# Performance work log

Hardware: AMD Instinct MI355X
Metric: run time of the kernel (lower is better)

## Reference

```python
import jax, jax.numpy as jnp
import numpy as np

N, E, G = 50000, 800000, 512
D_IN, HID, E_DIM = 128, 128, 128
NEG_SLOPE = 0.2


def setup_inputs() -> dict:
    key = jax.random.key(0)
    ks = iter(jax.random.split(key, 40))
    nrm = lambda shape, s: jax.random.normal(next(ks), shape, jnp.float32) * s
    lin = lambda i, o: nrm((i, o), 1.0 / np.sqrt(i))
    inp = {
        "x": jax.random.randint(next(ks), (N, 9), 0, 119),
        "edge_index": jax.random.randint(next(ks), (2, E), 0, N),
        "edge_attr": jax.random.randint(next(ks), (E, 3), 0, 5),
        "batch": jnp.sort(jax.random.randint(next(ks), (N,), 0, G)),
        # OGB-style encoders: sum of per-feature embeddings
        "atom_emb": nrm((9, 128, D_IN), 0.1),
        "bond_emb": nrm((3, 8, E_DIM), 0.1),
        # GATv2 layer 1 (in=D_IN)
        "W1l": lin(D_IN, HID), "b1l": jnp.zeros((HID,), jnp.float32),
        "W1r": lin(D_IN, HID), "b1r": jnp.zeros((HID,), jnp.float32),
        "W1e": lin(E_DIM, HID), "att1": nrm((HID,), 1.0 / np.sqrt(HID)),
        "bias1": jnp.zeros((HID,), jnp.float32),
        # GATv2 layer 2 (in=HID)
        "W2l": lin(HID, HID), "b2l": jnp.zeros((HID,), jnp.float32),
        "W2r": lin(HID, HID), "b2r": jnp.zeros((HID,), jnp.float32),
        "W2e": lin(E_DIM, HID), "att2": nrm((HID,), 1.0 / np.sqrt(HID)),
        "bias2": jnp.zeros((HID,), jnp.float32),
        # readout linear
        "Wout": lin(HID, 1), "bout": jnp.zeros((1,), jnp.float32),
    }
    return inp


def _segment_softmax(scores, seg, n):
    m = jax.ops.segment_max(scores, seg, num_segments=n)
    ex = jnp.exp(scores - m[seg])
    s = jax.ops.segment_sum(ex, seg, num_segments=n)
    return ex / s[seg]


def _add_self_loops(edge_index, edge_attr):
    # PyG add_self_loops with fill_value='mean': loop attr = mean of incoming edge_attr
    dst = edge_index[1]
    cnt = jax.ops.segment_sum(jnp.ones((E,), edge_attr.dtype), dst, num_segments=N)
    mean_attr = jax.ops.segment_sum(edge_attr, dst, num_segments=N) / jnp.maximum(cnt, 1.0)[:, None]
    loop = jnp.arange(N)
    ei = jnp.concatenate([edge_index, jnp.stack([loop, loop])], axis=1)
    ea = jnp.concatenate([edge_attr, mean_attr], axis=0)
    return ei, ea


def _gatv2(h, src, dst, e_emb, Wl, bl, Wr, br, We, att, bias):
    hl = h @ Wl + bl                      # [N, HID] source transform
    hr = h @ Wr + br                      # [N, HID] target transform
    z = jax.nn.leaky_relu(hl[src] + hr[dst] + e_emb @ We, NEG_SLOPE)  # [E', HID]
    alpha = _segment_softmax(z @ att, dst, N)                          # [E']
    out = jax.ops.segment_sum(alpha[:, None] * hl[src], dst, num_segments=N)
    return out + bias


def reference(x, edge_index, edge_attr, batch, atom_emb, bond_emb,
              W1l, b1l, W1r, b1r, W1e, att1, bias1,
              W2l, b2l, W2r, b2r, W2e, att2, bias2, Wout, bout):
    # encoders: sum of per-feature embedding lookups
    h = jnp.sum(atom_emb[jnp.arange(9)[None, :], x], axis=1)        # [N, D_IN]
    ea = jnp.sum(bond_emb[jnp.arange(3)[None, :], edge_attr], axis=1)  # [E, E_DIM]
    ei, ea = _add_self_loops(edge_index, ea)
    src, dst = ei[0], ei[1]
    h = _gatv2(h, src, dst, ea, W1l, b1l, W1r, b1r, W1e, att1, bias1)
    h = jax.nn.relu(h)
    h = _gatv2(h, src, dst, ea, W2l, b2l, W2r, b2r, W2e, att2, bias2)
    # global mean pool over graphs
    cnt = jax.ops.segment_sum(jnp.ones((N,), h.dtype), batch, num_segments=G)
    g = jax.ops.segment_sum(h, batch, num_segments=G) / jnp.maximum(cnt, 1.0)[:, None]
    # dropout is identity in eval mode
    return jax.nn.sigmoid(g @ Wout + bout)                           # [G, 1]
```

## Files before the change

### kernel.cpp

```cpp
#include <hip/hip_runtime.h>
#include <hip/hip_bf16.h>
#include <math.h>


typedef unsigned int uint;

#define THREADS 256
#define LOG2E 1.4426950408889634f
#define SRC_MASK 0x7fffffu

__global__ void atom_kernel(const int* __restrict__ x, const float* __restrict__ atom_emb,
                            float* __restrict__ h, int n) {
  int idx = blockIdx.x * blockDim.x + threadIdx.x;
  int node = idx >> 7, d = idx & 127;
  if (node >= n) return;
  float s = 0.f;
#pragma unroll
  for (int f = 0; f < 9; f++) {
    int v = x[node * 9 + f];
    s += atom_emb[(f * 128 + v) * 128 + d];
  }
  h[idx] = s;
}

__global__ void edge_hist_kernel(const int* __restrict__ ei, const int* __restrict__ ea,
                                 uint* __restrict__ cnt, uint* __restrict__ hist, int E_) {
  int e = blockIdx.x * blockDim.x + threadIdx.x;
  if (e >= E_) return;
  int dst = ei[E_ + e];
  int a0 = ea[e * 3 + 0], a1 = ea[e * 3 + 1], a2 = ea[e * 3 + 2];
  atomicAdd(&cnt[dst], 1u);
  atomicAdd(&hist[dst * 24 + a0], 1u);
  atomicAdd(&hist[dst * 24 + 8 + a1], 1u);
  atomicAdd(&hist[dst * 24 + 16 + a2], 1u);
}

__global__ __launch_bounds__(256) void scanA_kernel(const uint* __restrict__ cnt,
                                                    uint* __restrict__ off,
                                                    uint* __restrict__ bsum, int n) {
  __shared__ uint sc[256];
  int t = threadIdx.x;
  int base = blockIdx.x * 1024 + t * 4;
  uint v[4];
#pragma unroll
  for (int i = 0; i < 4; i++) v[i] = (base + i < n) ? cnt[base + i] : 0u;
  uint s = v[0] + v[1] + v[2] + v[3];
  sc[t] = s;
  __syncthreads();
  for (int o = 1; o < 256; o <<= 1) {
    uint w = (t >= o) ? sc[t - o] : 0u;
    __syncthreads();
    sc[t] += w;
    __syncthreads();
  }
  uint excl = sc[t] - s;
  uint r = excl;
#pragma unroll
  for (int i = 0; i < 4; i++) {
    if (base + i < n) off[base + i] = r;
    r += v[i];
  }
  if (t == 255) bsum[blockIdx.x] = sc[t];
}

__global__ __launch_bounds__(256) void scanB_kernel(const uint* __restrict__ bsum,
                                                    uint* __restrict__ bpre, int nb) {
  __shared__ uint sc[256];
  int t = threadIdx.x;
  uint s = (t < nb) ? bsum[t] : 0u;
  sc[t] = s;
  __syncthreads();
  for (int o = 1; o < 256; o <<= 1) {
    uint w = (t >= o) ? sc[t - o] : 0u;
    __syncthreads();
    sc[t] += w;
    __syncthreads();
  }
  if (t < nb) bpre[t] = sc[t] - s;
}

__global__ void scanC_kernel(uint* __restrict__ off, const uint* __restrict__ bpre, int n,
                             int E_) {
  int i = blockIdx.x * blockDim.x + threadIdx.x;
  if (i < n) off[i] += bpre[i >> 10];
  if (i == 0) off[n] = (uint)E_;
}

__global__ void scatter_kernel(const int* __restrict__ ei, const int* __restrict__ ea,
                               const uint* __restrict__ off, uint* __restrict__ fill,
                               uint* __restrict__ sorted, int E_) {
  int e = blockIdx.x * blockDim.x + threadIdx.x;
  if (e >= E_) return;
  int src = ei[e], dst = ei[E_ + e];
  uint pos = off[dst] + atomicAdd(&fill[dst], 1u);
  uint pk = ((uint)src & SRC_MASK) | ((uint)ea[e * 3 + 0] << 23) |
            ((uint)ea[e * 3 + 1] << 26) | ((uint)ea[e * 3 + 2] << 29);
  sorted[pos] = pk;
}

__global__ void table_kernel(const float* __restrict__ bond_emb, const float* __restrict__ W1e,
                             const float* __restrict__ W2e, float* __restrict__ tab1,
                             float* __restrict__ tab2) {
  __shared__ float row[128];
  int b = blockIdx.x;
  int j = (b < 24) ? b : b - 24;
  const float* We = (b < 24) ? W1e : W2e;
  float* tab = (b < 24) ? tab1 : tab2;
  row[threadIdx.x] = bond_emb[j * 128 + threadIdx.x];
  __syncthreads();
  float acc = 0.f;
#pragma unroll 4
  for (int k = 0; k < 128; k++) acc += row[k] * We[k * 128 + threadIdx.x];
  tab[j * 128 + threadIdx.x] = acc;
}

__global__ __launch_bounds__(256) void lin2_kernel(
    const float* __restrict__ h, const float* __restrict__ Wl, const float* __restrict__ bl,
    const float* __restrict__ Wr, const float* __restrict__ br,
    float* __restrict__ hl, float* __restrict__ hr, int n) {
  __shared__ float hs[32][132];
  int r0 = blockIdx.x * 32;
  for (int i = threadIdx.x; i < 32 * 128; i += 256) {
    int r = i >> 7, c = i & 127;
    int gr = r0 + r;
    hs[r][c] = (gr < n) ? h[gr * 128 + c] : 0.f;
  }
  __syncthreads();
  int col = threadIdx.x & 127;
  int half = threadIdx.x >> 7;
  float accl[16], accr[16];
  float bvl = bl[col], bvr = br[col];
#pragma unroll
  for (int i = 0; i < 16; i++) { accl[i] = bvl; accr[i] = bvr; }
  for (int k = 0; k < 128; k += 4) {
    float wl[4], wr[4];
#pragma unroll
    for (int kk = 0; kk < 4; kk++) {
      wl[kk] = Wl[(k + kk) * 128 + col];
      wr[kk] = Wr[(k + kk) * 128 + col];
    }
#pragma unroll
    for (int i = 0; i < 16; i++) {
      float4 hv = *(const float4*)&hs[half * 16 + i][k];
      accl[i] += hv.x * wl[0] + hv.y * wl[1] + hv.z * wl[2] + hv.w * wl[3];
      accr[i] += hv.x * wr[0] + hv.y * wr[1] + hv.z * wr[2] + hv.w * wr[3];
    }
  }
#pragma unroll
  for (int i = 0; i < 16; i++) {
    int gr = r0 + half * 16 + i;
    if (gr < n) {
      hl[gr * 128 + col] = accl[i];
      hr[gr * 128 + col] = accr[i];
    }
  }
}

__global__ __launch_bounds__(256) void attn_kernel(
    const float* __restrict__ hl, const float* __restrict__ hr,
    const uint* __restrict__ off, const uint* __restrict__ sorted,
    const uint* __restrict__ cnt, const uint* __restrict__ hist,
    const float* __restrict__ tab, const float* __restrict__ att,
    const float* __restrict__ bias, float* __restrict__ out, int n, int do_relu) {
  __shared__ float tabs[24][128];
  __shared__ float atts[128];
  for (int i = threadIdx.x; i < 24 * 128; i += 256) tabs[i >> 7][i & 127] = tab[i];
  if (threadIdx.x < 128) atts[threadIdx.x] = att[threadIdx.x] * LOG2E;
  __syncthreads();
  int wave = threadIdx.x >> 6, lane = threadIdx.x & 63;
  int node = blockIdx.x * 4 + wave;
  if (node >= n) return;
  int d = lane * 2;

  float2 hrv = *(const float2*)&hr[node * 128 + d];
  float2 hlo = *(const float2*)&hl[node * 128 + d];
  float2 av = make_float2(atts[d], atts[d + 1]);

  float2 ep = make_float2(0.f, 0.f);
  uint c = cnt[node];
  if (c) {
#pragma unroll
    for (int j = 0; j < 24; j++) {
      float f = (float)hist[node * 24 + j];
      float2 tv = *(const float2*)&tabs[j][d];
      ep.x += f * tv.x;
      ep.y += f * tv.y;
    }
    float inv = 1.0f / (float)c;
    ep.x *= inv;
    ep.y *= inv;
  }

  auto score_of = [&](float2 hls, float2 epv) -> float {
    float tx = hls.x + hrv.x + epv.x;
    float ty = hls.y + hrv.y + epv.y;
    tx = tx > 0.f ? tx : 0.2f * tx;
    ty = ty > 0.f ? ty : 0.2f * ty;
    float p = tx * av.x + ty * av.y;
#pragma unroll
    for (int o = 32; o > 0; o >>= 1) p += __shfl_xor(p, o);
    return p;
  };
  auto eproj_of = [&](uint pk) -> float2 {
    int a0 = (pk >> 23) & 7, a1 = (pk >> 26) & 7, a2 = (pk >> 29) & 7;
    float2 t0 = *(const float2*)&tabs[a0][d];
    float2 t1 = *(const float2*)&tabs[8 + a1][d];
    float2 t2 = *(const float2*)&tabs[16 + a2][d];
    return make_float2(t0.x + t1.x + t2.x, t0.y + t1.y + t2.y);
  };

  float m = score_of(hlo, ep);
  float s = 1.0f;
  float2 acc = hlo;

  uint e0 = off[node], e1 = off[node + 1];
  for (uint e = e0; e < e1; e += 8) {
    uint pk[8];
    float2 hv[8];
    float sc[8], p[8];
#pragma unroll
    for (int i = 0; i < 8; i++) {
      uint ee = e + (uint)i;
      pk[i] = sorted[ee < e1 ? ee : e1 - 1];
    }
#pragma unroll
    for (int i = 0; i < 8; i++) hv[i] = *(const float2*)&hl[(pk[i] & SRC_MASK) * 128 + d];
#pragma unroll
    for (int i = 0; i < 8; i++) sc[i] = score_of(hv[i], eproj_of(pk[i]));
#pragma unroll
    for (int i = 0; i < 8; i++)
      if (e + (uint)i >= e1) sc[i] = -INFINITY;
    float m8 = sc[0];
#pragma unroll
    for (int i = 1; i < 8; i++) m8 = fmaxf(m8, sc[i]);
    float mn = fmaxf(m, m8);
    float corr = exp2f(m - mn);
#pragma unroll
    for (int i = 0; i < 8; i++) p[i] = exp2f(sc[i] - mn);
    float ps = 0.f;
    float2 pa = make_float2(0.f, 0.f);
#pragma unroll
    for (int i = 0; i < 8; i++) {
      ps += p[i];
      pa.x += p[i] * hv[i].x;
      pa.y += p[i] * hv[i].y;
    }
    s = s * corr + ps;
    acc.x = acc.x * corr + pa.x;
    acc.y = acc.y * corr + pa.y;
    m = mn;
  }

  float inv = 1.0f / s;
  float2 o;
  o.x = acc.x * inv + bias[d];
  o.y = acc.y * inv + bias[d + 1];
  if (do_relu) {
    o.x = fmaxf(o.x, 0.f);
    o.y = fmaxf(o.y, 0.f);
  }
  *(float2*)&out[node * 128 + d] = o;
}

#define POOL_CHUNK 128
__global__ void pool_kernel(const float* __restrict__ h, const int* __restrict__ batch,
                            float* __restrict__ pool, uint* __restrict__ cntg, int n) {
  int d = threadIdx.x;
  int i0 = blockIdx.x * POOL_CHUNK;
  if (i0 >= n) return;
  int i1 = min(i0 + POOL_CHUNK, n);
  int g = batch[i0];
  float s = 0.f;
  uint c = 0;
  for (int i = i0; i < i1; i++) {
    int gi = batch[i];
    if (gi != g) {
      atomicAdd(&pool[g * 128 + d], s);
      if (d == 0) atomicAdd(&cntg[g], c);
      g = gi;
      s = 0.f;
      c = 0;
    }
    s += h[i * 128 + d];
    c++;
  }
  atomicAdd(&pool[g * 128 + d], s);
  if (d == 0) atomicAdd(&cntg[g], c);
}

__global__ void out_kernel(const float* __restrict__ pool, const uint* __restrict__ cntg,
                           const float* __restrict__ Wout, const float* __restrict__ bout,
                           float* __restrict__ out, int g_) {
  int wave = threadIdx.x >> 6, lane = threadIdx.x & 63;
  int g = blockIdx.x * 4 + wave;
  if (g >= g_) return;
  int d = lane * 2;
  float2 pv = *(const float2*)&pool[g * 128 + d];
  float2 wv = *(const float2*)&Wout[d];
  float p = pv.x * wv.x + pv.y * wv.y;
#pragma unroll
  for (int o = 32; o > 0; o >>= 1) p += __shfl_xor(p, o);
  if (lane == 0) {
    uint c = cntg[g];
    float cf = (float)(c ? c : 1u);
    float v = p / cf + bout[0];
    out[g] = 1.f / (1.f + expf(-v));
  }
}

extern "C" void kernel_launch(void* const* d_in, const int* in_sizes, int n_in,
                              void* d_out, int out_size, void* d_ws, size_t ws_size,
                              hipStream_t stream) {
  const int* x          = (const int*)d_in[0];
  const int* edge_index = (const int*)d_in[1];
  const int* edge_attr  = (const int*)d_in[2];
  const int* batch      = (const int*)d_in[3];
  const float* atom_emb = (const float*)d_in[4];
  const float* bond_emb = (const float*)d_in[5];
  const float* W1l = (const float*)d_in[6];
  const float* b1l = (const float*)d_in[7];
  const float* W1r = (const float*)d_in[8];
  const float* b1r = (const float*)d_in[9];
  const float* W1e = (const float*)d_in[10];
  const float* att1 = (const float*)d_in[11];
  const float* bias1 = (const float*)d_in[12];
  const float* W2l = (const float*)d_in[13];
  const float* b2l = (const float*)d_in[14];
  const float* W2r = (const float*)d_in[15];
  const float* b2r = (const float*)d_in[16];
  const float* W2e = (const float*)d_in[17];
  const float* att2 = (const float*)d_in[18];
  const float* bias2 = (const float*)d_in[19];
  const float* Wout = (const float*)d_in[20];
  const float* bout = (const float*)d_in[21];
  float* out = (float*)d_out;

  const int N = in_sizes[0] / 9;
  const int E = in_sizes[1] / 2;
  const int G = out_size;
  const int NB = (N + 1023) / 1024;

  char* w = (char*)d_ws;
  auto alloc = [&](size_t bytes) -> char* {
    char* p = w;
    w += (bytes + 255) & ~(size_t)255;
    return p;
  };
  float* h0     = (float*)alloc((size_t)N * 128 * 4);
  float* hl     = (float*)alloc((size_t)N * 128 * 4);
  float* hr     = (float*)alloc((size_t)N * 128 * 4);
  uint* cnt     = (uint*)alloc((size_t)N * 4);
  uint* off     = (uint*)alloc((size_t)(N + 1) * 4);
  uint* fill    = (uint*)alloc((size_t)N * 4);
  uint* hist    = (uint*)alloc((size_t)N * 24 * 4);
  uint* sorted  = (uint*)alloc((size_t)E * 4);
  float* tab1   = (float*)alloc(24 * 128 * 4);
  float* tab2   = (float*)alloc(24 * 128 * 4);
  float* pool   = (float*)alloc((size_t)G * 128 * 4);
  uint* cntg    = (uint*)alloc((size_t)G * 4);
  uint* bsum    = (uint*)alloc((size_t)NB * 4);
  uint* bpre    = (uint*)alloc((size_t)NB * 4);

  hipMemsetAsync(cnt, 0, (size_t)N * 4, stream);
  hipMemsetAsync(fill, 0, (size_t)N * 4, stream);
  hipMemsetAsync(hist, 0, (size_t)N * 24 * 4, stream);
  hipMemsetAsync(pool, 0, (size_t)G * 128 * 4, stream);
  hipMemsetAsync(cntg, 0, (size_t)G * 4, stream);

  table_kernel<<<48, 128, 0, stream>>>(bond_emb, W1e, W2e, tab1, tab2);
  atom_kernel<<<(N * 128 + THREADS - 1) / THREADS, THREADS, 0, stream>>>(x, atom_emb, h0, N);
  edge_hist_kernel<<<(E + THREADS - 1) / THREADS, THREADS, 0, stream>>>(edge_index, edge_attr,
                                                                        cnt, hist, E);
  scanA_kernel<<<NB, 256, 0, stream>>>(cnt, off, bsum, N);
  scanB_kernel<<<1, 256, 0, stream>>>(bsum, bpre, NB);
  scanC_kernel<<<(N + THREADS - 1) / THREADS, THREADS, 0, stream>>>(off, bpre, N, E);
  scatter_kernel<<<(E + THREADS - 1) / THREADS, THREADS, 0, stream>>>(edge_index, edge_attr, off,
                                                                      fill, sorted, E);
  lin2_kernel<<<(N + 31) / 32, 256, 0, stream>>>(h0, W1l, b1l, W1r, b1r, hl, hr, N);
  attn_kernel<<<(N + 3) / 4, 256, 0, stream>>>(hl, hr, off, sorted, cnt, hist, tab1, att1, bias1,
                                               h0, N, 1);
  lin2_kernel<<<(N + 31) / 32, 256, 0, stream>>>(h0, W2l, b2l, W2r, b2r, hl, hr, N);
  attn_kernel<<<(N + 3) / 4, 256, 0, stream>>>(hl, hr, off, sorted, cnt, hist, tab2, att2, bias2,
                                               h0, N, 0);
  pool_kernel<<<(N + POOL_CHUNK - 1) / POOL_CHUNK, 128, 0, stream>>>(h0, batch, pool, cntg, N);
  out_kernel<<<(G + 3) / 4, 256, 0, stream>>>(pool, cntg, Wout, bout, out, G);
}
```

Baseline: 784.9 us.

## Split wavefront into four edge groups with float4 lanes in GATv2 attention

The attention kernel now splits each 64-lane wave into four 16-lane groups. Each group covers the 128 features with float4x2 per lane and handles a different edge, two per iteration. Partial online-softmax states are merged with cross-group shuffles at the end, which cuts the per-edge 64-lane reduction to four shuffle steps and widens the gathers. Separately, the in-degree count array and its atomics are dropped, and degree is recomputed from the attribute histogram. This adds a merge epilogue and more registers per lane.

Measured after the change: 727.7 us. 1.08x faster.

```diff
diff --git a/kernel.cpp b/kernel.cpp
--- a/kernel.cpp
+++ b/kernel.cpp
@@ -7,7 +7,29 @@
 
 #define THREADS 256
 #define LOG2E 1.4426950408889634f
+#define NEGM -1e30f
 #define SRC_MASK 0x7fffffu
+
+__device__ inline float4 f4add(float4 x, float4 y) {
+  return make_float4(x.x + y.x, x.y + y.y, x.z + y.z, x.w + y.w);
+}
+__device__ inline float4 f4fma(float c, float4 x, float4 y) {
+  return make_float4(fmaf(c, x.x, y.x), fmaf(c, x.y, y.y), fmaf(c, x.z, y.z),
+                     fmaf(c, x.w, y.w));
+}
+__device__ inline float4 f4scale(float4 x, float c) {
+  return make_float4(x.x * c, x.y * c, x.z * c, x.w * c);
+}
+__device__ inline float lrelu_dot(float4 z, float4 a) {
+  float r = (z.x > 0.f ? z.x : 0.2f * z.x) * a.x;
+  r += (z.y > 0.f ? z.y : 0.2f * z.y) * a.y;
+  r += (z.z > 0.f ? z.z : 0.2f * z.z) * a.z;
+  r += (z.w > 0.f ? z.w : 0.2f * z.w) * a.w;
+  return r;
+}
+__device__ inline float4 f4relu(float4 x) {
+  return make_float4(fmaxf(x.x, 0.f), fmaxf(x.y, 0.f), fmaxf(x.z, 0.f), fmaxf(x.w, 0.f));
+}
 
 __global__ void atom_kernel(const int* __restrict__ x, const float* __restrict__ atom_emb,
                             float* __restrict__ h, int n) {
@@ -24,18 +46,17 @@
 }
 
 __global__ void edge_hist_kernel(const int* __restrict__ ei, const int* __restrict__ ea,
-                                 uint* __restrict__ cnt, uint* __restrict__ hist, int E_) {
+                                 uint* __restrict__ hist, int E_) {
   int e = blockIdx.x * blockDim.x + threadIdx.x;
   if (e >= E_) return;
   int dst = ei[E_ + e];
   int a0 = ea[e * 3 + 0], a1 = ea[e * 3 + 1], a2 = ea[e * 3 + 2];
-  atomicAdd(&cnt[dst], 1u);
   atomicAdd(&hist[dst * 24 + a0], 1u);
   atomicAdd(&hist[dst * 24 + 8 + a1], 1u);
   atomicAdd(&hist[dst * 24 + 16 + a2], 1u);
 }
 
-__global__ __launch_bounds__(256) void scanA_kernel(const uint* __restrict__ cnt,
+__global__ __launch_bounds__(256) void scanA_kernel(const uint* __restrict__ hist,
                                                     uint* __restrict__ off,
                                                     uint* __restrict__ bsum, int n) {
   __shared__ uint sc[256];
@@ -43,7 +64,16 @@
   int base = blockIdx.x * 1024 + t * 4;
   uint v[4];
 #pragma unroll
-  for (int i = 0; i < 4; i++) v[i] = (base + i < n) ? cnt[base + i] : 0u;
+  for (int i = 0; i < 4; i++) {
+    uint d = 0;
+    int idx = base + i;
+    if (idx < n) {
+      const uint4* hp = (const uint4*)&hist[idx * 24];
+      uint4 h0 = hp[0], h1 = hp[1];
+      d = h0.x + h0.y + h0.z + h0.w + h1.x + h1.y + h1.z + h1.w;
+    }
+    v[i] = d;
+  }
   uint s = v[0] + v[1] + v[2] + v[3];
   sc[t] = s;
   __syncthreads();
@@ -53,8 +83,7 @@
     sc[t] += w;
     __syncthreads();
   }
-  uint excl = sc[t] - s;
-  uint r = excl;
+  uint r = sc[t] - s;
 #pragma unroll
   for (int i = 0; i < 4; i++) {
     if (base + i < n) off[base + i] = r;
@@ -159,107 +188,126 @@
 __global__ __launch_bounds__(256) void attn_kernel(
     const float* __restrict__ hl, const float* __restrict__ hr,
     const uint* __restrict__ off, const uint* __restrict__ sorted,
-    const uint* __restrict__ cnt, const uint* __restrict__ hist,
-    const float* __restrict__ tab, const float* __restrict__ att,
-    const float* __restrict__ bias, float* __restrict__ out, int n, int do_relu) {
+    const uint* __restrict__ hist, const float* __restrict__ tab,
+    const float* __restrict__ att, const float* __restrict__ bias,
+    float* __restrict__ out, int n, int do_relu) {
   __shared__ float tabs[24][128];
-  __shared__ float atts[128];
   for (int i = threadIdx.x; i < 24 * 128; i += 256) tabs[i >> 7][i & 127] = tab[i];
-  if (threadIdx.x < 128) atts[threadIdx.x] = att[threadIdx.x] * LOG2E;
   __syncthreads();
   int wave = threadIdx.x >> 6, lane = threadIdx.x & 63;
   int node = blockIdx.x * 4 + wave;
   if (node >= n) return;
-  int d = lane * 2;
-
-  float2 hrv = *(const float2*)&hr[node * 128 + d];
-  float2 hlo = *(const float2*)&hl[node * 128 + d];
-  float2 av = make_float2(atts[d], atts[d + 1]);
-
-  float2 ep = make_float2(0.f, 0.f);
-  uint c = cnt[node];
+  int g = lane >> 4;
+  int dq = (lane & 15) * 8;
+
+  const float* hrp = &hr[(size_t)node * 128 + dq];
+  const float* hlp = &hl[(size_t)node * 128 + dq];
+  float4 hr0 = *(const float4*)hrp, hr1 = *(const float4*)(hrp + 4);
+  float4 hl0 = *(const float4*)hlp, hl1 = *(const float4*)(hlp + 4);
+  float4 at0 = f4scale(*(const float4*)&att[dq], LOG2E);
+  float4 at1 = f4scale(*(const float4*)&att[dq + 4], LOG2E);
+
+  float4 ep0 = make_float4(0.f, 0.f, 0.f, 0.f), ep1 = ep0;
+  uint c = 0;
+#pragma unroll
+  for (int j = 0; j < 24; j++) {
+    uint hc = hist[node * 24 + j];
+    if (j < 8) c += hc;
+    if (hc) {
+      float f = (float)hc;
+      ep0 = f4fma(f, *(const float4*)&tabs[j][dq], ep0);
+      ep1 = f4fma(f, *(const float4*)&tabs[j][dq + 4], ep1);
+    }
+  }
   if (c) {
-#pragma unroll
-    for (int j = 0; j < 24; j++) {
-      float f = (float)hist[node * 24 + j];
-      float2 tv = *(const float2*)&tabs[j][d];
-      ep.x += f * tv.x;
-      ep.y += f * tv.y;
-    }
-    float inv = 1.0f / (float)c;
-    ep.x *= inv;
-    ep.y *= inv;
-  }
-
-  auto score_of = [&](float2 hls, float2 epv) -> float {
-    float tx = hls.x + hrv.x + epv.x;
-    float ty = hls.y + hrv.y + epv.y;
-    tx = tx > 0.f ? tx : 0.2f * tx;
-    ty = ty > 0.f ? ty : 0.2f * ty;
-    float p = tx * av.x + ty * av.y;
-#pragma unroll
-    for (int o = 32; o > 0; o >>= 1) p += __shfl_xor(p, o);
+    float ic = 1.f / (float)c;
+    ep0 = f4scale(ep0, ic);
+    ep1 = f4scale(ep1, ic);
+  }
+
+  auto redscore = [&](float4 z0, float4 z1) -> float {
+    float p = lrelu_dot(z0, at0) + lrelu_dot(z1, at1);
+    p += __shfl_xor(p, 1);
+    p += __shfl_xor(p, 2);
+    p += __shfl_xor(p, 4);
+    p += __shfl_xor(p, 8);
     return p;
   };
-  auto eproj_of = [&](uint pk) -> float2 {
-    int a0 = (pk >> 23) & 7, a1 = (pk >> 26) & 7, a2 = (pk >> 29) & 7;
-    float2 t0 = *(const float2*)&tabs[a0][d];
-    float2 t1 = *(const float2*)&tabs[8 + a1][d];
-    float2 t2 = *(const float2*)&tabs[16 + a2][d];
-    return make_float2(t0.x + t1.x + t2.x, t0.y + t1.y + t2.y);
-  };
-
-  float m = score_of(hlo, ep);
-  float s = 1.0f;
-  float2 acc = hlo;
+
+  float sself = redscore(f4add(f4add(hl0, hr0), ep0), f4add(f4add(hl1, hr1), ep1));
+
+  float m, s;
+  float4 a0, a1;
+  if (g == 0) {
+    m = sself; s = 1.f; a0 = hl0; a1 = hl1;
+  } else {
+    m = NEGM; s = 0.f;
+    a0 = make_float4(0.f, 0.f, 0.f, 0.f); a1 = a0;
+  }
 
   uint e0 = off[node], e1 = off[node + 1];
-  for (uint e = e0; e < e1; e += 8) {
-    uint pk[8];
-    float2 hv[8];
-    float sc[8], p[8];
-#pragma unroll
-    for (int i = 0; i < 8; i++) {
-      uint ee = e + (uint)i;
-      pk[i] = sorted[ee < e1 ? ee : e1 - 1];
-    }
-#pragma unroll
-    for (int i = 0; i < 8; i++) hv[i] = *(const float2*)&hl[(pk[i] & SRC_MASK) * 128 + d];
-#pragma unroll
-    for (int i = 0; i < 8; i++) sc[i] = score_of(hv[i], eproj_of(pk[i]));
-#pragma unroll
-    for (int i = 0; i < 8; i++)
-      if (e + (uint)i >= e1) sc[i] = -INFINITY;
-    float m8 = sc[0];
-#pragma unroll
-    for (int i = 1; i < 8; i++) m8 = fmaxf(m8, sc[i]);
-    float mn = fmaxf(m, m8);
+  for (uint base = e0; base < e1; base += 8) {
+    uint eA = base + (uint)g, eB = eA + 4u;
+    uint iA = eA < e1 ? eA : e1 - 1;
+    uint iB = eB < e1 ? eB : e1 - 1;
+    uint pkA = sorted[iA], pkB = sorted[iB];
+    const float* pa = &hl[(size_t)(pkA & SRC_MASK) * 128 + dq];
+    const float* pb = &hl[(size_t)(pkB & SRC_MASK) * 128 + dq];
+    float4 hA0 = *(const float4*)pa, hA1 = *(const float4*)(pa + 4);
+    float4 hB0 = *(const float4*)pb, hB1 = *(const float4*)(pb + 4);
+    int a0A = (pkA >> 23) & 7, a1A = (pkA >> 26) & 7, a2A = (pkA >> 29) & 7;
+    int a0B = (pkB >> 23) & 7, a1B = (pkB >> 26) & 7, a2B = (pkB >> 29) & 7;
+    float4 eA0 = f4add(f4add(*(const float4*)&tabs[a0A][dq], *(const float4*)&tabs[8 + a1A][dq]),
+                       *(const float4*)&tabs[16 + a2A][dq]);
+    float4 eA1 = f4add(f4add(*(const float4*)&tabs[a0A][dq + 4],
+                             *(const float4*)&tabs[8 + a1A][dq + 4]),
+                       *(const float4*)&tabs[16 + a2A][dq + 4]);
+    float4 eB0 = f4add(f4add(*(const float4*)&tabs[a0B][dq], *(const float4*)&tabs[8 + a1B][dq]),
+                       *(const float4*)&tabs[16 + a2B][dq]);
+    float4 eB1 = f4add(f4add(*(const float4*)&tabs[a0B][dq + 4],
+                             *(const float4*)&tabs[8 + a1B][dq + 4]),
+                       *(const float4*)&tabs[16 + a2B][dq + 4]);
+    float scA = redscore(f4add(f4add(hA0, hr0), eA0), f4add(f4add(hA1, hr1), eA1));
+    float scB = redscore(f4add(f4add(hB0, hr0), eB0), f4add(f4add(hB1, hr1), eB1));
+    if (eA >= e1) scA = NEGM;
+    if (eB >= e1) scB = NEGM;
+    float mn = fmaxf(m, fmaxf(scA, scB));
     float corr = exp2f(m - mn);
-#pragma unroll
-    for (int i = 0; i < 8; i++) p[i] = exp2f(sc[i] - mn);
-    float ps = 0.f;
-    float2 pa = make_float2(0.f, 0.f);
-#pragma unroll
-    for (int i = 0; i < 8; i++) {
-      ps += p[i];
-      pa.x += p[i] * hv[i].x;
-      pa.y += p[i] * hv[i].y;
-    }
-    s = s * corr + ps;
-    acc.x = acc.x * corr + pa.x;
-    acc.y = acc.y * corr + pa.y;
+    float pA = exp2f(scA - mn), pB = exp2f(scB - mn);
+    s = s * corr + pA + pB;
+    a0 = f4fma(pA, hA0, f4fma(pB, hB0, f4scale(a0, corr)));
+    a1 = f4fma(pA, hA1, f4fma(pB, hB1, f4scale(a1, corr)));
     m = mn;
   }
 
-  float inv = 1.0f / s;
-  float2 o;
-  o.x = acc.x * inv + bias[d];
-  o.y = acc.y * inv + bias[d + 1];
+#pragma unroll
+  for (int lvl = 16; lvl <= 32; lvl <<= 1) {
+    float om = __shfl_xor(m, lvl);
+    float os = __shfl_xor(s, lvl);
+    float4 o0 = make_float4(__shfl_xor(a0.x, lvl), __shfl_xor(a0.y, lvl),
+                            __shfl_xor(a0.z, lvl), __shfl_xor(a0.w, lvl));
+    float4 o1 = make_float4(__shfl_xor(a1.x, lvl), __shfl_xor(a1.y, lvl),
+                            __shfl_xor(a1.z, lvl), __shfl_xor(a1.w, lvl));
+    float mn = fmaxf(m, om);
+    float ca = exp2f(m - mn), cb = exp2f(om - mn);
+    s = s * ca + os * cb;
+    a0 = f4fma(cb, o0, f4scale(a0, ca));
+    a1 = f4fma(cb, o1, f4scale(a1, ca));
+    m = mn;
+  }
+
+  float inv = 1.f / s;
+  float4 b0 = *(const float4*)&bias[dq], b1 = *(const float4*)&bias[dq + 4];
+  float4 o0 = f4fma(inv, a0, b0);
+  float4 o1 = f4fma(inv, a1, b1);
   if (do_relu) {
-    o.x = fmaxf(o.x, 0.f);
-    o.y = fmaxf(o.y, 0.f);
-  }
-  *(float2*)&out[node * 128 + d] = o;
+    o0 = f4relu(o0);
+    o1 = f4relu(o1);
+  }
+  if (lane < 16) {
+    *(float4*)&out[(size_t)node * 128 + dq] = o0;
+    *(float4*)&out[(size_t)node * 128 + dq + 4] = o1;
+  }
 }
 
 #define POOL_CHUNK 128
@@ -349,7 +397,6 @@
   float* h0     = (float*)alloc((size_t)N * 128 * 4);
   float* hl     = (float*)alloc((size_t)N * 128 * 4);
   float* hr     = (float*)alloc((size_t)N * 128 * 4);
-  uint* cnt     = (uint*)alloc((size_t)N * 4);
   uint* off     = (uint*)alloc((size_t)(N + 1) * 4);
   uint* fill    = (uint*)alloc((size_t)N * 4);
   uint* hist    = (uint*)alloc((size_t)N * 24 * 4);
@@ -361,7 +408,6 @@
   uint* bsum    = (uint*)alloc((size_t)NB * 4);
   uint* bpre    = (uint*)alloc((size_t)NB * 4);
 
-  hipMemsetAsync(cnt, 0, (size_t)N * 4, stream);
   hipMemsetAsync(fill, 0, (size_t)N * 4, stream);
   hipMemsetAsync(hist, 0, (size_t)N * 24 * 4, stream);
   hipMemsetAsync(pool, 0, (size_t)G * 128 * 4, stream);
@@ -370,17 +416,17 @@
   table_kernel<<<48, 128, 0, stream>>>(bond_emb, W1e, W2e, tab1, tab2);
   atom_kernel<<<(N * 128 + THREADS - 1) / THREADS, THREADS, 0, stream>>>(x, atom_emb, h0, N);
   edge_hist_kernel<<<(E + THREADS - 1) / THREADS, THREADS, 0, stream>>>(edge_index, edge_attr,
-                                                                        cnt, hist, E);
-  scanA_kernel<<<NB, 256, 0, stream>>>(cnt, off, bsum, N);
+                                                                        hist, E);
+  scanA_kernel<<<NB, 256, 0, stream>>>(hist, off, bsum, N);
   scanB_kernel<<<1, 256, 0, stream>>>(bsum, bpre, NB);
   scanC_kernel<<<(N + THREADS - 1) / THREADS, THREADS, 0, stream>>>(off, bpre, N, E);
   scatter_kernel<<<(E + THREADS - 1) / THREADS, THREADS, 0, stream>>>(edge_index, edge_attr, off,
                                                                       fill, sorted, E);
   lin2_kernel<<<(N + 31) / 32, 256, 0, stream>>>(h0, W1l, b1l, W1r, b1r, hl, hr, N);
-  attn_kernel<<<(N + 3) / 4, 256, 0, stream>>>(hl, hr, off, sorted, cnt, hist, tab1, att1, bias1,
+  attn_kernel<<<(N + 3) / 4, 256, 0, stream>>>(hl, hr, off, sorted, hist, tab1, att1, bias1,
                                                h0, N, 1);
   lin2_kernel<<<(N + 31) / 32, 256, 0, stream>>>(h0, W2l, b2l, W2r, b2r, hl, hr, N);
-  attn_kernel<<<(N + 3) / 4, 256, 0, stream>>>(hl, hr, off, sorted, cnt, hist, tab2, att2, bias2,
+  attn_kernel<<<(N + 3) / 4, 256, 0, stream>>>(hl, hr, off, sorted, hist, tab2, att2, bias2,
                                                h0, N, 0);
   pool_kernel<<<(N + POOL_CHUNK - 1) / POOL_CHUNK, 128, 0, stream>>>(h0, batch, pool, cntg, N);
   out_kernel<<<(G + 3) / 4, 256, 0, stream>>>(pool, cntg, Wout, bout, out, G);
```
